# Performance work log

Hardware: AMD Instinct MI355X
Metric: run time of the kernel (lower is better)

## Reference

```python
import jax, jax.numpy as jnp
import numpy as np

B, L, V, D = 16, 1024, 10000, 512
DG, DX = 256, 256
LAM = 0.5
EPS = 1e-5


def setup_inputs() -> dict:
    key = jax.random.key(0)
    ks = jax.random.split(key, 16)
    s = 0.02
    return {
        "tokens": jax.random.randint(ks[0], (B, L), 0, V),
        "emb": jax.random.normal(ks[1], (V, D), jnp.float32) * s,
        "W_ih": jax.random.normal(ks[2], (3 * D, D), jnp.float32) * s,
        "W_hh": jax.random.normal(ks[3], (3 * D, D), jnp.float32) * s,
        "b_ih": jnp.zeros((3 * D,), jnp.float32),
        "b_hh": jnp.zeros((3 * D,), jnp.float32),
        "Wg": jax.random.normal(ks[4], (DG, D), jnp.float32) * s,
        "bg": jnp.zeros((DG,), jnp.float32),
        "Wx": jax.random.normal(ks[5], (DX, D), jnp.float32) * s,
        "bx": jnp.zeros((DX,), jnp.float32),
        "Wp": jax.random.normal(ks[6], (DX, D), jnp.float32) * s,
        "bp": jnp.zeros((DX,), jnp.float32),
        "ln_g": jnp.ones((DX,), jnp.float32),
        "ln_b": jnp.zeros((DX,), jnp.float32),
        "Wo": jax.random.normal(ks[7], (V, DX), jnp.float32) * s,
        "bo": jnp.zeros((V,), jnp.float32),
    }


def _layernorm(x, g, b):
    mu = jnp.mean(x, -1, keepdims=True)
    var = jnp.var(x, -1, keepdims=True)
    return (x - mu) * jax.lax.rsqrt(var + EPS) * g + b


def reference(tokens, emb, W_ih, W_hh, b_ih, b_hh, Wg, bg, Wx, bx, Wp, bp, ln_g, ln_b, Wo, bo):
    e = emb[tokens]                       # (B, L, D)
    e_t = jnp.transpose(e, (1, 0, 2))      # (L, B, D) for scan

    def step(carry, et):
        h, M = carry                       # h: (B,D), M: (B,DG,DX)
        gi = et @ W_ih.T + b_ih            # (B, 3D)
        gh = h @ W_hh.T + b_hh
        i_r, i_z, i_n = jnp.split(gi, 3, axis=-1)
        h_r, h_z, h_n = jnp.split(gh, 3, axis=-1)
        r = jax.nn.sigmoid(i_r + h_r)
        z = jax.nn.sigmoid(i_z + h_z)
        n = jnp.tanh(i_n + r * h_n)
        h_new = (1.0 - z) * n + z * h
        g = h_new @ Wg.T + bg              # (B, DG)
        x = h_new @ Wx.T + bx              # (B, DX)
        xp = h_new @ Wp.T + bp             # (B, DX)
        retr = jnp.einsum('bg,bgx->bx', g, M)  # read from M_{t-1}
        x_hat = (1.0 - LAM) * xp + LAM * retr
        logits = _layernorm(x_hat, ln_g, ln_b) @ Wo.T + bo
        M_new = M + g[:, :, None] * x[:, None, :]  # Hebbian outer-product write
        return (h_new, M_new), logits

    h0 = jnp.zeros((B, D), e.dtype)
    M0 = jnp.zeros((B, DG, DX), e.dtype)
    _, logits = jax.lax.scan(step, (h0, M0), e_t)
    return jnp.transpose(logits, (1, 0, 2))  # (B, L, V)
```

## Files before the change

### kernel.cpp

```cpp
#include <hip/hip_runtime.h>

#define L_SEQ 1024
#define B_SZ  16
#define D_SZ  512
#define V_SZ  10000
#define HQ_DEPTH 32
#define REC_DEPTH 64
#define WSTR 536
#define PW_T 272
#define PW_WAVE 1632
#define PW_BUF 6528

typedef __attribute__((ext_vector_type(8))) short bf16x8;
typedef __attribute__((ext_vector_type(4))) float f32x4;
typedef __attribute__((ext_vector_type(4))) unsigned int u32x4;
typedef __attribute__((ext_vector_type(2))) unsigned int u32x2;

__device__ __forceinline__ float bf2f(unsigned int u) {
  unsigned int x = (u & 0xffffu) << 16;
  return __builtin_bit_cast(float, x);
}
__device__ __forceinline__ unsigned short f2bf(float f) {
  unsigned int x = __builtin_bit_cast(unsigned int, f);
  x += 0x7fffu + ((x >> 16) & 1u);
  return (unsigned short)(x >> 16);
}
__device__ __forceinline__ unsigned int pk2(float lo, float hi) {
  return (unsigned int)f2bf(lo) | ((unsigned int)f2bf(hi) << 16);
}
__device__ __forceinline__ float sigm(float x) { return 1.f / (1.f + __expf(-x)); }
__device__ __forceinline__ float tanhfast(float x) {
  x = fminf(fmaxf(x, -15.f), 15.f);
  float e = __expf(2.f * x);
  return (e - 1.f) / (e + 1.f);
}

#define KPAD 40

__global__ __launch_bounds__(256) void k_gi(
    const int* __restrict__ tokens, const float* __restrict__ emb,
    const float* __restrict__ Wih, const float* __restrict__ bih,
    unsigned short* __restrict__ giT)
{
  __shared__ unsigned short As[64 * KPAD];
  __shared__ unsigned short Bs[64 * KPAD];
  const int tid = threadIdx.x, lane = tid & 63, wv = tid >> 6;
  const int m0 = blockIdx.y * 64, n0 = blockIdx.x * 64;
  const int sr = tid >> 2, skc = (tid & 3) * 8;
  const int grow = m0 + sr;
  const int tok = tokens[((grow & 15) << 10) + (grow >> 4)];
  const float* asrc = emb + (size_t)tok * 512 + skc;
  const float* bsrc = Wih + (size_t)(n0 + sr) * 512 + skc;

  f32x4 acc[4];
  #pragma unroll
  for (int i = 0; i < 4; ++i) acc[i] = 0.f;

  for (int ks = 0; ks < 16; ++ks) {
    __syncthreads();
    float4 a0 = *(const float4*)(asrc + ks * 32);
    float4 a1 = *(const float4*)(asrc + ks * 32 + 4);
    float4 q0 = *(const float4*)(bsrc + ks * 32);
    float4 q1 = *(const float4*)(bsrc + ks * 32 + 4);
    uint4 ua = { pk2(a0.x, a0.y), pk2(a0.z, a0.w), pk2(a1.x, a1.y), pk2(a1.z, a1.w) };
    uint4 ub = { pk2(q0.x, q0.y), pk2(q0.z, q0.w), pk2(q1.x, q1.y), pk2(q1.z, q1.w) };
    *(uint4*)&As[sr * KPAD + skc] = ua;
    *(uint4*)&Bs[sr * KPAD + skc] = ub;
    __syncthreads();
    bf16x8 af = *(const bf16x8*)&As[(wv * 16 + (lane & 15)) * KPAD + (lane >> 4) * 8];
    #pragma unroll
    for (int ns = 0; ns < 4; ++ns) {
      bf16x8 bfv = *(const bf16x8*)&Bs[(ns * 16 + (lane & 15)) * KPAD + (lane >> 4) * 8];
      acc[ns] = __builtin_amdgcn_mfma_f32_16x16x32_bf16(af, bfv, acc[ns], 0, 0, 0);
    }
  }
  const int mrow = m0 + wv * 16 + 4 * (lane >> 4);
  const int ncol = n0 + (lane & 15);
  #pragma unroll
  for (int ns = 0; ns < 4; ++ns) {
    int col = ncol + ns * 16;
    float bv = bih[col];
    #pragma unroll
    for (int rr = 0; rr < 4; ++rr) {
      int row = mrow + rr;
      giT[((size_t)(row >> 4) * 1536 + col) * 16 + (row & 15)] = f2bf(acc[ns][rr] + bv);
    }
  }
}

__global__ __launch_bounds__(256) void k_scan(
    const unsigned short* __restrict__ giT,
    const float* __restrict__ Whh, const float* __restrict__ bhh,
    const float* __restrict__ Wg, const float* __restrict__ bg,
    const float* __restrict__ Wx, const float* __restrict__ bx,
    const float* __restrict__ Wp, const float* __restrict__ bp,
    u32x4* __restrict__ recS, unsigned short* __restrict__ xhat,
    unsigned long long* __restrict__ hq)
{
  __shared__ char smem[155136];
  const int tid = threadIdx.x;
  const int lane = tid & 63, v = tid >> 6;
  const int wid = blockIdx.x;

  if (wid < 24) {
    const bool isGH = (wid < 16);
    const int w = isGH ? wid : (wid - 16);
    unsigned short* wlds = (unsigned short*)smem;
    float* pscr = (float*)(smem + 102912);

    for (int row = v; row < 96; row += 4) {
      const float* src;
      if (isGH) {
        src = Whh + ((size_t)(row >> 5) * 512 + w * 32 + (row & 31)) * 512;
      } else {
        int m = row >> 5;
        const float* Wm = (m == 0) ? Wg : (m == 1) ? Wx : Wp;
        src = Wm + (size_t)(w * 32 + (row & 31)) * 512;
      }
      float4 p0 = *(const float4*)(src + lane * 8);
      float4 p1 = *(const float4*)(src + lane * 8 + 4);
      uint4 uu = { pk2(p0.x, p0.y), pk2(p0.z, p0.w), pk2(p1.x, p1.y), pk2(p1.z, p1.w) };
      *(uint4*)&wlds[row * WSTR + lane * 8] = uu;
    }
    __syncthreads();

    const int b_ = lane & 15, hi = lane >> 4;
    const int bbh = tid & 15, dph = tid >> 4;
    const int bbx = tid >> 4, dpx = tid & 15;

    float bhr1 = 0, bhz1 = 0, bhn1 = 0, bhr2 = 0, bhz2 = 0, bhn2 = 0;
    float bgc0 = 0, bgc1 = 0, bxc0 = 0, bxc1 = 0, bpc0 = 0, bpc1 = 0;
    float hprev1 = 0.f, hprev2 = 0.f;
    if (isGH) {
      int d0 = w * 32 + 2 * dph, d1 = d0 + 1;
      bhr1 = bhh[d0]; bhz1 = bhh[512 + d0]; bhn1 = bhh[1024 + d0];
      bhr2 = bhh[d1]; bhz2 = bhh[512 + d1]; bhn2 = bhh[1024 + d1];
    } else {
      int d0 = w * 32 + 2 * dpx, d1 = d0 + 1;
      bgc0 = bg[d0]; bgc1 = bg[d1];
      bxc0 = bx[d0]; bxc1 = bx[d1];
      bpc0 = bp[d0]; bpc1 = bp[d1];
    }

    float gir1 = 0, giz1 = 0, gin1 = 0, gir2 = 0, giz2 = 0, gin2 = 0;
    float nir1 = 0, niz1 = 0, nin1 = 0, nir2 = 0, niz2 = 0, nin2 = 0;
    if (isGH) {
      int d0 = w * 32 + 2 * dph, d1 = d0 + 1;
      const unsigned short* gib = giT + bbh;
      gir1 = bf2f(gib[(size_t)d0 * 16]);
      giz1 = bf2f(gib[(size_t)(512 + d0) * 16]);
      gin1 = bf2f(gib[(size_t)(1024 + d0) * 16]);
      gir2 = bf2f(gib[(size_t)d1 * 16]);
      giz2 = bf2f(gib[(size_t)(512 + d1) * 16]);
      gin2 = bf2f(gib[(size_t)(1024 + d1) * 16]);
    }

    const unsigned short* bqbase = wlds + (size_t)b_ * WSTR + (size_t)(4 * v) * 32 + hi * 8;

    #pragma unroll 1
    for (int t = 0; t < L_SEQ; ++t) {
      const int pt = isGH ? (t - 1) : t;
      f32x4 pacc[6];
      #pragma unroll
      for (int i = 0; i < 6; ++i) pacc[i] = 0.f;

      if (pt >= 0) {
        const unsigned long long* hsrc = hq + (size_t)(pt & (HQ_DEPTH - 1)) * 4096
                                            + (size_t)b_ * 256 + 64 * v + 4 * hi;
        const unsigned int tv = (unsigned int)(pt + 1);
        u32x4 q0, q1, q2, q3, q4, q5, q6, q7;
        int spins = 0;
        for (;;) {
          asm volatile(
            "global_load_dwordx4 %0, %8, off sc0 sc1\n\t"
            "global_load_dwordx4 %1, %8, off offset:16 sc0 sc1\n\t"
            "global_load_dwordx4 %2, %8, off offset:128 sc0 sc1\n\t"
            "global_load_dwordx4 %3, %8, off offset:144 sc0 sc1\n\t"
            "global_load_dwordx4 %4, %8, off offset:256 sc0 sc1\n\t"
            "global_load_dwordx4 %5, %8, off offset:272 sc0 sc1\n\t"
            "global_load_dwordx4 %6, %8, off offset:384 sc0 sc1\n\t"
            "global_load_dwordx4 %7, %8, off offset:400 sc0 sc1\n\t"
            "s_waitcnt vmcnt(0)"
            : "=&v"(q0), "=&v"(q1), "=&v"(q2), "=&v"(q3),
              "=&v"(q4), "=&v"(q5), "=&v"(q6), "=&v"(q7)
            : "v"(hsrc) : "memory");
          bool ok = (q0.y == tv) && (q0.w == tv) && (q1.y == tv) && (q1.w == tv)
                 && (q2.y == tv) && (q2.w == tv) && (q3.y == tv) && (q3.w == tv)
                 && (q4.y == tv) && (q4.w == tv) && (q5.y == tv) && (q5.w == tv)
                 && (q6.y == tv) && (q6.w == tv) && (q7.y == tv) && (q7.w == tv);
          if (__all(ok)) break;
          if (!isGH) __builtin_amdgcn_s_sleep(4);
          if (++spins > 2000000) break;
        }
        u32x4 f0 = { q0.x, q0.z, q1.x, q1.z };
        u32x4 f1 = { q2.x, q2.z, q3.x, q3.z };
        u32x4 f2 = { q4.x, q4.z, q5.x, q5.z };
        u32x4 f3 = { q6.x, q6.z, q7.x, q7.z };
        bf16x8 a0 = __builtin_bit_cast(bf16x8, f0);
        bf16x8 a1 = __builtin_bit_cast(bf16x8, f1);
        bf16x8 a2 = __builtin_bit_cast(bf16x8, f2);
        bf16x8 a3 = __builtin_bit_cast(bf16x8, f3);
        #pragma unroll
        for (int T = 0; T < 6; ++T) {
          const unsigned short* bp0 = bqbase + (size_t)T * (16 * WSTR);
          bf16x8 w0 = *(const bf16x8*)(bp0);
          bf16x8 w1 = *(const bf16x8*)(bp0 + 32);
          bf16x8 w2 = *(const bf16x8*)(bp0 + 64);
          bf16x8 w3 = *(const bf16x8*)(bp0 + 96);
          pacc[T] = __builtin_amdgcn_mfma_f32_16x16x32_bf16(a0, w0, pacc[T], 0, 0, 0);
          pacc[T] = __builtin_amdgcn_mfma_f32_16x16x32_bf16(a1, w1, pacc[T], 0, 0, 0);
          pacc[T] = __builtin_amdgcn_mfma_f32_16x16x32_bf16(a2, w2, pacc[T], 0, 0, 0);
          pacc[T] = __builtin_amdgcn_mfma_f32_16x16x32_bf16(a3, w3, pacc[T], 0, 0, 0);
        }
      }

      if (isGH && (t + 1 < L_SEQ)) {
        int d0 = w * 32 + 2 * dph, d1 = d0 + 1;
        const unsigned short* gib = giT + (size_t)(t + 1) * 1536 * 16 + bbh;
        nir1 = bf2f(gib[(size_t)d0 * 16]);
        niz1 = bf2f(gib[(size_t)(512 + d0) * 16]);
        nin1 = bf2f(gib[(size_t)(1024 + d0) * 16]);
        nir2 = bf2f(gib[(size_t)d1 * 16]);
        niz2 = bf2f(gib[(size_t)(512 + d1) * 16]);
        nin2 = bf2f(gib[(size_t)(1024 + d1) * 16]);
      }

      {
        float* pw = pscr + (size_t)(t & 1) * PW_BUF + (size_t)v * PW_WAVE;
        #pragma unroll
        for (int T = 0; T < 6; ++T) {
          #pragma unroll
          for (int rr = 0; rr < 4; ++rr)
            pw[T * PW_T + (4 * hi + rr) * 17 + b_] = pacc[T][rr];
        }
      }
      __syncthreads();

      const float* pb = pscr + (size_t)(t & 1) * PW_BUF;
      if (isGH) {
        const int Tr = dph >> 3, j0 = (2 * dph) & 15;
        const int base0 = Tr * PW_T + bbh * 17 + j0;
        float ar1 = pb[base0]              + pb[PW_WAVE + base0]              + pb[2*PW_WAVE + base0]              + pb[3*PW_WAVE + base0];
        float ar2 = pb[base0 + 1]          + pb[PW_WAVE + base0 + 1]          + pb[2*PW_WAVE + base0 + 1]          + pb[3*PW_WAVE + base0 + 1];
        float az1 = pb[base0 + 2*PW_T]     + pb[PW_WAVE + base0 + 2*PW_T]     + pb[2*PW_WAVE + base0 + 2*PW_T]     + pb[3*PW_WAVE + base0 + 2*PW_T];
        float az2 = pb[base0 + 2*PW_T + 1] + pb[PW_WAVE + base0 + 2*PW_T + 1] + pb[2*PW_WAVE + base0 + 2*PW_T + 1] + pb[3*PW_WAVE + base0 + 2*PW_T + 1];
        float an1 = pb[base0 + 4*PW_T]     + pb[PW_WAVE + base0 + 4*PW_T]     + pb[2*PW_WAVE + base0 + 4*PW_T]     + pb[3*PW_WAVE + base0 + 4*PW_T];
        float an2 = pb[base0 + 4*PW_T + 1] + pb[PW_WAVE + base0 + 4*PW_T + 1] + pb[2*PW_WAVE + base0 + 4*PW_T + 1] + pb[3*PW_WAVE + base0 + 4*PW_T + 1];
        float r1 = sigm(ar1 + gir1 + bhr1);
        float z1 = sigm(az1 + giz1 + bhz1);
        float n1 = tanhfast(gin1 + r1 * (an1 + bhn1));
        float h1 = (1.f - z1) * n1 + z1 * hprev1; hprev1 = h1;
        float r2 = sigm(ar2 + gir2 + bhr2);
        float z2 = sigm(az2 + giz2 + bhz2);
        float n2 = tanhfast(gin2 + r2 * (an2 + bhn2));
        float h2 = (1.f - z2) * n2 + z2 * hprev2; hprev2 = h2;
        u32x2 hv = { pk2(h1, h2), (unsigned int)(t + 1) };
        unsigned long long* hdst = hq + (size_t)(t & (HQ_DEPTH - 1)) * 4096
                                      + (size_t)bbh * 256 + w * 16 + dph;
        asm volatile("global_store_dwordx2 %0, %1, off sc0 sc1" :: "v"(hdst), "v"(hv) : "memory");
        gir1 = nir1; giz1 = niz1; gin1 = nin1;
        gir2 = nir2; giz2 = niz2; gin2 = nin2;
      } else {
        const int Tg = dpx >> 3, j0 = (2 * dpx) & 15;
        const int base0 = Tg * PW_T + bbx * 17 + j0;
        float g0 = pb[base0]              + pb[PW_WAVE + base0]              + pb[2*PW_WAVE + base0]              + pb[3*PW_WAVE + base0];
        float g1 = pb[base0 + 1]          + pb[PW_WAVE + base0 + 1]          + pb[2*PW_WAVE + base0 + 1]          + pb[3*PW_WAVE + base0 + 1];
        float x0 = pb[base0 + 2*PW_T]     + pb[PW_WAVE + base0 + 2*PW_T]     + pb[2*PW_WAVE + base0 + 2*PW_T]     + pb[3*PW_WAVE + base0 + 2*PW_T];
        float x1 = pb[base0 + 2*PW_T + 1] + pb[PW_WAVE + base0 + 2*PW_T + 1] + pb[2*PW_WAVE + base0 + 2*PW_T + 1] + pb[3*PW_WAVE + base0 + 2*PW_T + 1];
        float p0 = pb[base0 + 4*PW_T]     + pb[PW_WAVE + base0 + 4*PW_T]     + pb[2*PW_WAVE + base0 + 4*PW_T]     + pb[3*PW_WAVE + base0 + 4*PW_T];
        float p1 = pb[base0 + 4*PW_T + 1] + pb[PW_WAVE + base0 + 4*PW_T + 1] + pb[2*PW_WAVE + base0 + 4*PW_T + 1] + pb[3*PW_WAVE + base0 + 4*PW_T + 1];
        g0 += bgc0; g1 += bgc1; x0 += bxc0; x1 += bxc1; p0 += bpc0; p1 += bpc1;
        u32x4 rec = { pk2(g0, g1), pk2(x0, x1), pk2(p0, p1), (unsigned int)(t + 1) };
        u32x4* rdst = recS + ((size_t)(t & (REC_DEPTH - 1)) * 16 + bbx) * 128 + w * 16 + dpx;
        asm volatile("global_store_dwordx4 %0, %1, off sc0 sc1" :: "v"(rdst), "v"(rec) : "memory");
      }
    }
  } else {
    const int id = wid - 24;
    const int b = id >> 1, sg = id & 1;
    const int sl = sg * 4 + v;
    float* Msh = (float*)(smem + v * 32768);
    const int colg = lane & 7, dgs = lane >> 3;
    for (int i = lane * 4; i < 8192; i += 256) *(float4*)&Msh[i] = float4{0.f, 0.f, 0.f, 0.f};
    #pragma unroll 1
    for (int t = 0; t < L_SEQ; ++t) {
      const u32x4* rp = recS + ((size_t)(t & (REC_DEPTH - 1)) * 16 + b) * 128 + 2 * lane;
      const unsigned int tagv = (unsigned int)(t + 1);
      u32x4 r0, r1;
      int spins = 0;
      for (;;) {
        asm volatile(
          "global_load_dwordx4 %0, %2, off sc0 sc1\n\t"
          "global_load_dwordx4 %1, %2, off offset:16 sc0 sc1\n\t"
          "s_waitcnt vmcnt(0)"
          : "=&v"(r0), "=&v"(r1) : "v"(rp) : "memory");
        if (__all((r0.w == tagv) && (r1.w == tagv))) break;
        __builtin_amdgcn_s_sleep(8);
        if (++spins > 2000000) break;
      }
      const int lx = sl * 8 + colg;
      unsigned int xa = (unsigned int)__shfl((int)r0.y, lx);
      unsigned int xb = (unsigned int)__shfl((int)r1.y, lx);
      unsigned int pa = (unsigned int)__shfl((int)r0.z, lx);
      unsigned int pb2 = (unsigned int)__shfl((int)r1.z, lx);
      float xv0 = bf2f(xa), xv1 = bf2f(xa >> 16), xv2 = bf2f(xb), xv3 = bf2f(xb >> 16);
      float r0a = 0, r1a = 0, r2a = 0, r3a = 0;
      #pragma unroll
      for (int ic = 0; ic < 8; ++ic) {
        const int ls = dgs * 8 + ic;
        unsigned int ga = (unsigned int)__shfl((int)r0.x, ls);
        unsigned int gb = (unsigned int)__shfl((int)r1.x, ls);
        float gj[4] = { bf2f(ga), bf2f(ga >> 16), bf2f(gb), bf2f(gb >> 16) };
        int dg = dgs * 32 + ic * 4;
        #pragma unroll
        for (int j = 0; j < 4; ++j) {
          float4* mp = (float4*)&Msh[(dg + j) * 32 + colg * 4];
          float4 m = *mp;
          r0a += gj[j] * m.x; r1a += gj[j] * m.y; r2a += gj[j] * m.z; r3a += gj[j] * m.w;
          m.x += gj[j] * xv0; m.y += gj[j] * xv1; m.z += gj[j] * xv2; m.w += gj[j] * xv3;
          *mp = m;
        }
      }
      #pragma unroll
      for (int off = 8; off < 64; off <<= 1) {
        r0a += __shfl_xor(r0a, off); r1a += __shfl_xor(r1a, off);
        r2a += __shfl_xor(r2a, off); r3a += __shfl_xor(r3a, off);
      }
      if (dgs == 0) {
        float y0 = 0.5f * bf2f(pa) + 0.5f * r0a;
        float y1 = 0.5f * bf2f(pa >> 16) + 0.5f * r1a;
        float y2 = 0.5f * bf2f(pb2) + 0.5f * r2a;
        float y3 = 0.5f * bf2f(pb2 >> 16) + 0.5f * r3a;
        uint2 ou = { pk2(y0, y1), pk2(y2, y3) };
        *(uint2*)(xhat + ((size_t)t * 16 + b) * 256 + sl * 32 + colg * 4) = ou;
      }
    }
  }
}

__global__ __launch_bounds__(256) void k_ln(
    unsigned short* xh, const float* __restrict__ g, const float* __restrict__ bta)
{
  int row = blockIdx.x * 4 + (threadIdx.x >> 6);
  int lane = threadIdx.x & 63;
  size_t base = (size_t)row * 256 + lane * 4;
  uint2 raw = *(const uint2*)(xh + base);
  float v0 = bf2f(raw.x), v1 = bf2f(raw.x >> 16), v2 = bf2f(raw.y), v3 = bf2f(raw.y >> 16);
  float s1 = v0 + v1 + v2 + v3;
  float s2 = v0 * v0 + v1 * v1 + v2 * v2 + v3 * v3;
  #pragma unroll
  for (int off = 1; off < 64; off <<= 1) { s1 += __shfl_xor(s1, off); s2 += __shfl_xor(s2, off); }
  float mu = s1 * (1.f / 256.f);
  float var = s2 * (1.f / 256.f) - mu * mu;
  float rs = rsqrtf(var + 1e-5f);
  int c = lane * 4;
  float y0 = (v0 - mu) * rs * g[c] + bta[c];
  float y1 = (v1 - mu) * rs * g[c + 1] + bta[c + 1];
  float y2 = (v2 - mu) * rs * g[c + 2] + bta[c + 2];
  float y3 = (v3 - mu) * rs * g[c + 3] + bta[c + 3];
  uint2 ou = { pk2(y0, y1), pk2(y2, y3) };
  *(uint2*)(xh + base) = ou;
}

__global__ __launch_bounds__(256) void k_logits(
    const unsigned short* __restrict__ ln, const float* __restrict__ Wo,
    const float* __restrict__ bo, float* __restrict__ out)
{
  __shared__ unsigned short As[64 * KPAD];
  __shared__ unsigned short Bs[64 * KPAD];
  const int tid = threadIdx.x, lane = tid & 63, wv = tid >> 6;
  const int m0 = blockIdx.y * 64, n0 = blockIdx.x * 64;
  const int sr = tid >> 2, skc = (tid & 3) * 8;
  const unsigned short* asrc = ln + (size_t)(m0 + sr) * 256 + skc;
  const int brow = n0 + sr;
  const bool bok = brow < V_SZ;
  const float* bsrc = Wo + (size_t)(bok ? brow : 0) * 256 + skc;

  f32x4 acc[4];
  #pragma unroll
  for (int i = 0; i < 4; ++i) acc[i] = 0.f;

  for (int ks = 0; ks < 8; ++ks) {
    __syncthreads();
    *(uint4*)&As[sr * KPAD + skc] = *(const uint4*)(asrc + ks * 32);
    uint4 ub = {0u, 0u, 0u, 0u};
    if (bok) {
      float4 q0 = *(const float4*)(bsrc + ks * 32);
      float4 q1 = *(const float4*)(bsrc + ks * 32 + 4);
      ub.x = pk2(q0.x, q0.y); ub.y = pk2(q0.z, q0.w);
      ub.z = pk2(q1.x, q1.y); ub.w = pk2(q1.z, q1.w);
    }
    *(uint4*)&Bs[sr * KPAD + skc] = ub;
    __syncthreads();
    bf16x8 af = *(const bf16x8*)&As[(wv * 16 + (lane & 15)) * KPAD + (lane >> 4) * 8];
    #pragma unroll
    for (int ns = 0; ns < 4; ++ns) {
      bf16x8 bfv = *(const bf16x8*)&Bs[(ns * 16 + (lane & 15)) * KPAD + (lane >> 4) * 8];
      acc[ns] = __builtin_amdgcn_mfma_f32_16x16x32_bf16(af, bfv, acc[ns], 0, 0, 0);
    }
  }
  const int mrow = m0 + wv * 16 + 4 * (lane >> 4);
  const int ncol = n0 + (lane & 15);
  #pragma unroll
  for (int ns = 0; ns < 4; ++ns) {
    int col = ncol + ns * 16;
    if (col < V_SZ) {
      float bv = bo[col];
      #pragma unroll
      for (int rr = 0; rr < 4; ++rr) {
        int row = mrow + rr;
        out[(size_t)(row & 15) * ((size_t)L_SEQ * V_SZ) + (size_t)(row >> 4) * V_SZ + col] =
            acc[ns][rr] + bv;
      }
    }
  }
}

extern "C" void kernel_launch(void* const* d_in, const int* in_sizes, int n_in,
                              void* d_out, int out_size, void* d_ws, size_t ws_size,
                              hipStream_t stream)
{
  const int*   tokens = (const int*)d_in[0];
  const float* emb    = (const float*)d_in[1];
  const float* Wih    = (const float*)d_in[2];
  const float* Whh    = (const float*)d_in[3];
  const float* bih    = (const float*)d_in[4];
  const float* bhh    = (const float*)d_in[5];
  const float* Wg     = (const float*)d_in[6];
  const float* bg     = (const float*)d_in[7];
  const float* Wx     = (const float*)d_in[8];
  const float* bx     = (const float*)d_in[9];
  const float* Wp     = (const float*)d_in[10];
  const float* bp     = (const float*)d_in[11];
  const float* lng    = (const float*)d_in[12];
  const float* lnb    = (const float*)d_in[13];
  const float* Wo     = (const float*)d_in[14];
  const float* bo     = (const float*)d_in[15];
  float* out = (float*)d_out;

  char* ws = (char*)d_ws;
  size_t off = 0;
  auto take = [&](size_t bytes) -> char* {
    char* p = ws + off;
    off += (bytes + 255) & ~(size_t)255;
    return p;
  };
  unsigned short* giT    = (unsigned short*)take((size_t)1024 * 1536 * 16 * 2);
  u32x4* recS            = (u32x4*)take((size_t)REC_DEPTH * 16 * 128 * 16);
  unsigned short* xhat   = (unsigned short*)take((size_t)1024 * 16 * 256 * 2);
  unsigned long long* hq = (unsigned long long*)take((size_t)HQ_DEPTH * 4096 * 8);
  if (off > ws_size) return;

  (void)hipMemsetAsync(recS, 0, (size_t)REC_DEPTH * 16 * 128 * 16, stream);
  (void)hipMemsetAsync(hq, 0, (size_t)HQ_DEPTH * 4096 * 8, stream);

  k_gi<<<dim3(24, 256), 256, 0, stream>>>(tokens, emb, Wih, bih, giT);
  k_scan<<<56, 256, 0, stream>>>(giT, Whh, bhh, Wg, bg, Wx, bx, Wp, bp,
                                 recS, xhat, hq);
  k_ln<<<4096, 256, 0, stream>>>(xhat, lng, lnb);
  k_logits<<<dim3(157, 256), 256, 0, stream>>>(xhat, Wo, bo, out);
}
```

Baseline: 4.137 ms.

## Double-buffer spin-poll loads for h queue and pad reduction scratch stride

The GH waves now poll the hidden-state queue with two alternating batches of loads kept in flight, so each check waits on only the older batch and the next poll is already issued. The barrier is replaced with explicit waitcnt plus s_barrier, and the next-step gi prefetch is moved after the barrier. The LDS partial-sum scratch row stride changes from 17 to 18 floats to alter the bank mapping. This adds extra memory traffic while spinning and needs a vmcnt(0) drain every step.

```diff
diff --git a/kernel.cpp b/kernel.cpp
--- a/kernel.cpp
+++ b/kernel.cpp
@@ -7,9 +7,9 @@
 #define HQ_DEPTH 32
 #define REC_DEPTH 64
 #define WSTR 536
-#define PW_T 272
-#define PW_WAVE 1632
-#define PW_BUF 6528
+#define PW_T 288
+#define PW_WAVE 1728
+#define PW_BUF 6912
 
 typedef __attribute__((ext_vector_type(8))) short bf16x8;
 typedef __attribute__((ext_vector_type(4))) float f32x4;
@@ -88,6 +88,26 @@
   }
 }
 
+#define ISSUE_BATCH(R0,R1,R2,R3,R4,R5,R6,R7,PTR)                       \
+  asm volatile(                                                        \
+    "global_load_dwordx4 %0, %8, off sc0 sc1\n\t"                      \
+    "global_load_dwordx4 %1, %8, off offset:16 sc0 sc1\n\t"            \
+    "global_load_dwordx4 %2, %8, off offset:128 sc0 sc1\n\t"           \
+    "global_load_dwordx4 %3, %8, off offset:144 sc0 sc1\n\t"           \
+    "global_load_dwordx4 %4, %8, off offset:256 sc0 sc1\n\t"           \
+    "global_load_dwordx4 %5, %8, off offset:272 sc0 sc1\n\t"           \
+    "global_load_dwordx4 %6, %8, off offset:384 sc0 sc1\n\t"           \
+    "global_load_dwordx4 %7, %8, off offset:400 sc0 sc1"               \
+    : "=&v"(R0), "=&v"(R1), "=&v"(R2), "=&v"(R3),                      \
+      "=&v"(R4), "=&v"(R5), "=&v"(R6), "=&v"(R7)                       \
+    : "v"(PTR) : "memory")
+
+#define TAGS_OK(R0,R1,R2,R3,R4,R5,R6,R7,TV)                            \
+  ((R0.y == TV) & (R0.w == TV) & (R1.y == TV) & (R1.w == TV) &         \
+   (R2.y == TV) & (R2.w == TV) & (R3.y == TV) & (R3.w == TV) &         \
+   (R4.y == TV) & (R4.w == TV) & (R5.y == TV) & (R5.w == TV) &         \
+   (R6.y == TV) & (R6.w == TV) & (R7.y == TV) & (R7.w == TV))
+
 __global__ __launch_bounds__(256) void k_scan(
     const unsigned short* __restrict__ giT,
     const float* __restrict__ Whh, const float* __restrict__ bhh,
@@ -97,7 +117,7 @@
     u32x4* __restrict__ recS, unsigned short* __restrict__ xhat,
     unsigned long long* __restrict__ hq)
 {
-  __shared__ char smem[155136];
+  __shared__ char smem[158208];
   const int tid = threadIdx.x;
   const int lane = tid & 63, v = tid >> 6;
   const int wid = blockIdx.x;
@@ -143,7 +163,6 @@
     }
 
     float gir1 = 0, giz1 = 0, gin1 = 0, gir2 = 0, giz2 = 0, gin2 = 0;
-    float nir1 = 0, niz1 = 0, nin1 = 0, nir2 = 0, niz2 = 0, nin2 = 0;
     if (isGH) {
       int d0 = w * 32 + 2 * dph, d1 = d0 + 1;
       const unsigned short* gib = giT + bbh;
@@ -157,6 +176,9 @@
 
     const unsigned short* bqbase = wlds + (size_t)b_ * WSTR + (size_t)(4 * v) * 32 + hi * 8;
 
+    u32x4 A0 = 0, A1 = 0, A2 = 0, A3 = 0, A4 = 0, A5 = 0, A6 = 0, A7 = 0;
+    u32x4 B0 = 0, B1 = 0, B2 = 0, B3 = 0, B4 = 0, B5 = 0, B6 = 0, B7 = 0;
+
     #pragma unroll 1
     for (int t = 0; t < L_SEQ; ++t) {
       const int pt = isGH ? (t - 1) : t;
@@ -168,34 +190,36 @@
         const unsigned long long* hsrc = hq + (size_t)(pt & (HQ_DEPTH - 1)) * 4096
                                             + (size_t)b_ * 256 + 64 * v + 4 * hi;
         const unsigned int tv = (unsigned int)(pt + 1);
-        u32x4 q0, q1, q2, q3, q4, q5, q6, q7;
-        int spins = 0;
-        for (;;) {
-          asm volatile(
-            "global_load_dwordx4 %0, %8, off sc0 sc1\n\t"
-            "global_load_dwordx4 %1, %8, off offset:16 sc0 sc1\n\t"
-            "global_load_dwordx4 %2, %8, off offset:128 sc0 sc1\n\t"
-            "global_load_dwordx4 %3, %8, off offset:144 sc0 sc1\n\t"
-            "global_load_dwordx4 %4, %8, off offset:256 sc0 sc1\n\t"
-            "global_load_dwordx4 %5, %8, off offset:272 sc0 sc1\n\t"
-            "global_load_dwordx4 %6, %8, off offset:384 sc0 sc1\n\t"
-            "global_load_dwordx4 %7, %8, off offset:400 sc0 sc1\n\t"
-            "s_waitcnt vmcnt(0)"
-            : "=&v"(q0), "=&v"(q1), "=&v"(q2), "=&v"(q3),
-              "=&v"(q4), "=&v"(q5), "=&v"(q6), "=&v"(q7)
-            : "v"(hsrc) : "memory");
-          bool ok = (q0.y == tv) && (q0.w == tv) && (q1.y == tv) && (q1.w == tv)
-                 && (q2.y == tv) && (q2.w == tv) && (q3.y == tv) && (q3.w == tv)
-                 && (q4.y == tv) && (q4.w == tv) && (q5.y == tv) && (q5.w == tv)
-                 && (q6.y == tv) && (q6.w == tv) && (q7.y == tv) && (q7.w == tv);
-          if (__all(ok)) break;
-          if (!isGH) __builtin_amdgcn_s_sleep(4);
-          if (++spins > 2000000) break;
+        bool useA = true;
+        if (isGH) {
+          int spins = 0;
+          ISSUE_BATCH(A0, A1, A2, A3, A4, A5, A6, A7, hsrc);
+          for (;;) {
+            ISSUE_BATCH(B0, B1, B2, B3, B4, B5, B6, B7, hsrc);
+            asm volatile("s_waitcnt vmcnt(8)" ::: "memory");
+            if (__all(TAGS_OK(A0, A1, A2, A3, A4, A5, A6, A7, tv))) { useA = true; break; }
+            if (++spins > 1000000) { useA = true; break; }
+            ISSUE_BATCH(A0, A1, A2, A3, A4, A5, A6, A7, hsrc);
+            asm volatile("s_waitcnt vmcnt(8)" ::: "memory");
+            if (__all(TAGS_OK(B0, B1, B2, B3, B4, B5, B6, B7, tv))) { useA = false; break; }
+            if (++spins > 1000000) { useA = false; break; }
+          }
+        } else {
+          int spins = 0;
+          for (;;) {
+            ISSUE_BATCH(A0, A1, A2, A3, A4, A5, A6, A7, hsrc);
+            asm volatile("s_waitcnt vmcnt(0)" ::: "memory");
+            if (__all(TAGS_OK(A0, A1, A2, A3, A4, A5, A6, A7, tv))) break;
+            __builtin_amdgcn_s_sleep(4);
+            if (++spins > 1000000) break;
+          }
         }
-        u32x4 f0 = { q0.x, q0.z, q1.x, q1.z };
-        u32x4 f1 = { q2.x, q2.z, q3.x, q3.z };
-        u32x4 f2 = { q4.x, q4.z, q5.x, q5.z };
-        u32x4 f3 = { q6.x, q6.z, q7.x, q7.z };
+        u32x4 s0 = useA ? A0 : B0, s1 = useA ? A1 : B1, s2 = useA ? A2 : B2, s3 = useA ? A3 : B3;
+        u32x4 s4 = useA ? A4 : B4, s5 = useA ? A5 : B5, s6 = useA ? A6 : B6, s7 = useA ? A7 : B7;
+        u32x4 f0 = { s0.x, s0.z, s1.x, s1.z };
+        u32x4 f1 = { s2.x, s2.z, s3.x, s3.z };
+        u32x4 f2 = { s4.x, s4.z, s5.x, s5.z };
+        u32x4 f3 = { s6.x, s6.z, s7.x, s7.z };
         bf16x8 a0 = __builtin_bit_cast(bf16x8, f0);
         bf16x8 a1 = __builtin_bit_cast(bf16x8, f1);
         bf16x8 a2 = __builtin_bit_cast(bf16x8, f2);
@@ -214,6 +238,25 @@
         }
       }
 
+      {
+        float* pw = pscr + (size_t)(t & 1) * PW_BUF + (size_t)v * PW_WAVE;
+        #pragma unroll
+        for (int T = 0; T < 6; ++T) {
+          #pragma unroll
+          for (int rr = 0; rr < 4; ++rr)
+            pw[T * PW_T + (4 * hi + rr) * 18 + b_] = pacc[T][rr];
+        }
+      }
+      asm volatile("s_waitcnt lgkmcnt(0)" ::: "memory");
+      __builtin_amdgcn_s_barrier();
+      __builtin_amdgcn_sched_barrier(0);
+      asm volatile("s_waitcnt vmcnt(0)" ::: "memory");
+      __builtin_amdgcn_sched_barrier(0);
+      asm volatile("" :: "v"(A0), "v"(A1), "v"(A2), "v"(A3), "v"(A4), "v"(A5),
+                         "v"(A6), "v"(A7), "v"(B0), "v"(B1), "v"(B2), "v"(B3),
+                         "v"(B4), "v"(B5), "v"(B6), "v"(B7));
+
+      float nir1 = 0, niz1 = 0, nin1 = 0, nir2 = 0, niz2 = 0, nin2 = 0;
       if (isGH && (t + 1 < L_SEQ)) {
         int d0 = w * 32 + 2 * dph, d1 = d0 + 1;
         const unsigned short* gib = giT + (size_t)(t + 1) * 1536 * 16 + bbh;
@@ -225,21 +268,10 @@
         nin2 = bf2f(gib[(size_t)(1024 + d1) * 16]);
       }
 
-      {
-        float* pw = pscr + (size_t)(t & 1) * PW_BUF + (size_t)v * PW_WAVE;
-        #pragma unroll
-        for (int T = 0; T < 6; ++T) {
-          #pragma unroll
-          for (int rr = 0; rr < 4; ++rr)
-            pw[T * PW_T + (4 * hi + rr) * 17 + b_] = pacc[T][rr];
-        }
-      }
-      __syncthreads();
-
       const float* pb = pscr + (size_t)(t & 1) * PW_BUF;
       if (isGH) {
         const int Tr = dph >> 3, j0 = (2 * dph) & 15;
-        const int base0 = Tr * PW_T + bbh * 17 + j0;
+        const int base0 = Tr * PW_T + bbh * 18 + j0;
         float ar1 = pb[base0]              + pb[PW_WAVE + base0]              + pb[2*PW_WAVE + base0]              + pb[3*PW_WAVE + base0];
         float ar2 = pb[base0 + 1]          + pb[PW_WAVE + base0 + 1]          + pb[2*PW_WAVE + base0 + 1]          + pb[3*PW_WAVE + base0 + 1];
         float az1 = pb[base0 + 2*PW_T]     + pb[PW_WAVE + base0 + 2*PW_T]     + pb[2*PW_WAVE + base0 + 2*PW_T]     + pb[3*PW_WAVE + base0 + 2*PW_T];
@@ -262,7 +294,7 @@
         gir2 = nir2; giz2 = niz2; gin2 = nin2;
       } else {
         const int Tg = dpx >> 3, j0 = (2 * dpx) & 15;
-        const int base0 = Tg * PW_T + bbx * 17 + j0;
+        const int base0 = Tg * PW_T + bbx * 18 + j0;
         float g0 = pb[base0]              + pb[PW_WAVE + base0]              + pb[2*PW_WAVE + base0]              + pb[3*PW_WAVE + base0];
         float g1 = pb[base0 + 1]          + pb[PW_WAVE + base0 + 1]          + pb[2*PW_WAVE + base0 + 1]          + pb[3*PW_WAVE + base0 + 1];
         float x0 = pb[base0 + 2*PW_T]     + pb[PW_WAVE + base0 + 2*PW_T]     + pb[2*PW_WAVE + base0 + 2*PW_T]     + pb[3*PW_WAVE + base0 + 2*PW_T];
```

After: 6.295 ms. 52.2% more time.
